# Kernel optimization log

Hardware: AMD Instinct MI355X
Metric: run time of the kernel (lower is better)

## Reference

```python
import jax, jax.numpy as jnp
import numpy as np

B, N, IN, OUT, H = 256, 131, 512, 1024, 4
D = OUT // H  # head_dim
EDGE_SCALE = D ** -0.5
NODE_SCALE = OUT ** -0.5

lrelu = lambda x: jax.nn.leaky_relu(x, negative_slope=0.01)


def _glorot(key, shape):
    fan_in = shape[-1]
    return jax.random.normal(key, shape, dtype=jnp.float32) * (1.0 / np.sqrt(fan_in))


def setup_inputs() -> dict:
    key = jax.random.key(0)
    ks = jax.random.split(key, 16)
    return {
        "tabular_feats": jax.random.normal(ks[0], (B, 1, IN), dtype=jnp.float32),
        "node_feats": jax.random.normal(ks[1], (B, N, IN), dtype=jnp.float32),
        "adj_matrix": jax.random.uniform(ks[2], (B, N, N), dtype=jnp.float32),
        "W_gx": _glorot(ks[3], (OUT, IN)), "b_gx": jnp.zeros((OUT,), jnp.float32),
        "W_tx": _glorot(ks[4], (OUT, IN)), "b_tx": jnp.zeros((OUT,), jnp.float32),
        "W_gk": _glorot(ks[5], (OUT, IN)),
        "W_tq": _glorot(ks[6], (OUT, IN)),
        "W_gq": _glorot(ks[7], (OUT, IN)),
        "W_gs": _glorot(ks[8], (1, N)), "b_gs": jnp.zeros((1,), jnp.float32),
        "W_zx": _glorot(ks[9], (OUT, 2 * OUT)), "b_zx": jnp.zeros((OUT,), jnp.float32),
    }


def preprocess_adj(A):
    # add self-loops then symmetric degree normalization D^{-1/2} (A+I) D^{-1/2}
    A = A + jnp.eye(A.shape[-1], dtype=A.dtype)
    d_inv = jax.lax.rsqrt(jnp.sum(A, axis=-1))  # [b,h,x]
    return d_inv[..., :, None] * A * d_inv[..., None, :]


def reference(tabular_feats, node_feats, adj_matrix,
              W_gx, b_gx, W_tx, b_tx, W_gk, W_tq, W_gq, W_gs, b_gs, W_zx, b_zx):
    G_X = lrelu(node_feats @ W_gx.T + b_gx)            # [B,N,OUT]
    T_X = lrelu(tabular_feats @ W_tx.T + b_tx)         # [B,1,OUT]
    G_k = lrelu(node_feats @ W_gk.T)                   # [B,N,OUT]
    T_q = lrelu(tabular_feats @ W_tq.T)                # [B,1,OUT]

    node_att = jax.nn.softmax(jnp.einsum('bxh,byh->bxy', T_q, G_k) * NODE_SCALE, axis=-1)
    node_att = jnp.swapaxes(node_att + 1.0, -1, -2)    # [B,N,1]
    G_X = node_att * G_X                               # [B,N,OUT]

    G_X_mh = G_X.reshape(B, N, H, D).transpose(0, 2, 1, 3)            # [B,H,N,D]
    G_q_mh = lrelu(node_feats @ W_gq.T).reshape(B, N, H, D).transpose(0, 2, 1, 3)
    G_k_mh = G_k.reshape(B, N, H, D).transpose(0, 2, 1, 3)

    edge_att = jax.nn.sigmoid(jnp.einsum('bhxd,bhyd->bhxy', G_q_mh, G_k_mh) * EDGE_SCALE)
    adj_heads = adj_matrix[:, None] * edge_att         # [B,H,N,N]
    A = preprocess_adj(adj_heads)

    G_X = jnp.einsum('bhxy,bhyd->bhxd', A, G_X_mh).transpose(0, 2, 1, 3).reshape(B, N, OUT)

    # Graph_summary: Linear(num_node -> 1) over the node axis
    global_node = lrelu(jnp.einsum('bno,n->bo', G_X, W_gs[0]) + b_gs)  # [B,OUT]
    Z_in = jnp.concatenate([global_node, T_X.reshape(B, -1)], axis=-1)  # [B,2*OUT]
    Z_x = lrelu(Z_in @ W_zx.T + b_zx)                  # [B,OUT]
    return (G_X, T_X, Z_x, node_att, edge_att)
```

## Files before the change

### kernel.cpp

```cpp
#include <hip/hip_runtime.h>
#include <hip/hip_bf16.h>
#include <math.h>


#define LRELU(x) ((x) > 0.f ? (x) : 0.01f * (x))

constexpr int Bb = 256;
constexpr int Nn = 131;
constexpr int INF_ = 512;
constexpr int OUTF = 1024;
constexpr int Hh = 4;
constexpr int Dd = 256;
constexpr int OC2 = 2048;
constexpr int YP = 168;
constexpr int WLP = 174;
constexpr int KAGG = 160;

typedef __attribute__((ext_vector_type(8))) short bf16x8;
typedef __attribute__((ext_vector_type(4))) float f32x4;

__device__ __forceinline__ float bf2f(short s) {
    union { float f; unsigned u; } c;
    c.u = ((unsigned)(unsigned short)s) << 16;
    return c.f;
}

__device__ __forceinline__ void gload_lds16(const void* g, void* lds) {
    __builtin_amdgcn_global_load_lds(
        (const __attribute__((address_space(1))) void*)g,
        (__attribute__((address_space(3))) void*)lds, 16, 0, 0);
}

__global__ __launch_bounds__(256) void convert_kernel(
    const float* __restrict__ node, const float* __restrict__ Wgx,
    const float* __restrict__ Wgk, const float* __restrict__ Wgq,
    __hip_bfloat16* __restrict__ node_bf, __hip_bfloat16* __restrict__ Wcat)
{
    const size_t NE = (size_t)Bb * Nn * INF_ / 4;
    const size_t WE = (size_t)3072 * INF_ / 4;
    for (size_t i = (size_t)blockIdx.x * 256 + threadIdx.x; i < NE + WE;
         i += (size_t)gridDim.x * 256) {
        if (i < NE) {
            const float4 v = ((const float4*)node)[i];
            __hip_bfloat16* o = node_bf + i * 4;
            o[0] = __float2bfloat16(v.x); o[1] = __float2bfloat16(v.y);
            o[2] = __float2bfloat16(v.z); o[3] = __float2bfloat16(v.w);
        } else {
            const size_t j = i - NE;
            const size_t which = j / (1024 * INF_ / 4);
            const float* src = (which == 0) ? Wgk : (which == 1 ? Wgq : Wgx);
            const size_t srcj = j - which * (1024 * INF_ / 4);
            const float4 v = ((const float4*)src)[srcj];
            __hip_bfloat16* o = Wcat + j * 4;
            o[0] = __float2bfloat16(v.x); o[1] = __float2bfloat16(v.y);
            o[2] = __float2bfloat16(v.z); o[3] = __float2bfloat16(v.w);
        }
    }
}

__global__ __launch_bounds__(256, 4) void gemm_node_mfma(
    const __hip_bfloat16* __restrict__ A, const __hip_bfloat16* __restrict__ W,
    const float* __restrict__ bias_gx, const float* __restrict__ Tq,
    __hip_bfloat16* __restrict__ Gcat, __hip_bfloat16* __restrict__ GrawT,
    float* __restrict__ spart)
{
    __shared__ short SM[16384];
    short* As = SM;
    short* Bs = SM + 8192;
    const int tid = threadIdx.x;
    const int wave = tid >> 6, lane = tid & 63;
    const int m0 = blockIdx.y * 128, o0 = blockIdx.x * 128;
    const int wr = wave >> 1, wc = wave & 1;

    f32x4 acc[4][4] = {};
    const short* Asrc = (const short*)A;
    const short* Wsrc = (const short*)W;
    const int gsrc = ((tid & 7) ^ ((tid >> 3) & 7)) * 8;
    const int srow = tid >> 3;

    for (int kt = 0; kt < 8; ++kt) {
        const int k0 = kt * 64;
        #pragma unroll
        for (int j = 0; j < 4; ++j) {
            const int row = j * 32 + srow;
            gload_lds16(Asrc + (size_t)(m0 + row) * INF_ + k0 + gsrc,
                        &As[(j * 256 + (tid & ~63)) * 8]);
            gload_lds16(Wsrc + (size_t)(o0 + row) * INF_ + k0 + gsrc,
                        &Bs[(j * 256 + (tid & ~63)) * 8]);
        }
        __syncthreads();
        #pragma unroll
        for (int ks = 0; ks < 2; ++ks) {
            const int sa = ((ks * 4 + (lane >> 4)) ^ (lane & 7)) * 8;
            bf16x8 af[4], bfr[4];
            #pragma unroll
            for (int i = 0; i < 4; ++i) {
                af[i]  = *(const bf16x8*)&As[(wr * 64 + i * 16 + (lane & 15)) * 64 + sa];
                bfr[i] = *(const bf16x8*)&Bs[(wc * 64 + i * 16 + (lane & 15)) * 64 + sa];
            }
            #pragma unroll
            for (int mi = 0; mi < 4; ++mi)
                #pragma unroll
                for (int ni = 0; ni < 4; ++ni)
                    acc[mi][ni] = __builtin_amdgcn_mfma_f32_16x16x32_bf16(
                        af[mi], bfr[ni], acc[mi][ni], 0, 0, 0);
        }
        __syncthreads();
    }

    const int cc = lane & 15;
    const int rg = (lane >> 4) * 4;
    if (o0 < 1024) {
        const int blo = m0 / 131;
        const int msw = (blo + 1) * 131;
        float tqA[4], tqB[4];
        #pragma unroll
        for (int ni = 0; ni < 4; ++ni) {
            const int o = o0 + wc * 64 + ni * 16 + cc;
            tqA[ni] = Tq[(size_t)blo * OUTF + o];
            tqB[ni] = (blo + 1 < Bb) ? Tq[(size_t)(blo + 1) * OUTF + o] : 0.f;
        }
        float sc[4][4] = {};
        #pragma unroll
        for (int mi = 0; mi < 4; ++mi)
            #pragma unroll
            for (int ni = 0; ni < 4; ++ni) {
                const int o = o0 + wc * 64 + ni * 16 + cc;
                #pragma unroll
                for (int r = 0; r < 4; ++r) {
                    const int m = m0 + wr * 64 + mi * 16 + rg + r;
                    float v = acc[mi][ni][r];
                    v = LRELU(v);
                    Gcat[(size_t)m * OC2 + o] = __float2bfloat16(v);
                    sc[mi][r] += v * ((m >= msw) ? tqB[ni] : tqA[ni]);
                }
            }
        const int slot = (o0 >> 6) + wc;
        #pragma unroll
        for (int mi = 0; mi < 4; ++mi)
            #pragma unroll
            for (int r = 0; r < 4; ++r) {
                float s = sc[mi][r];
                s += __shfl_xor(s, 1); s += __shfl_xor(s, 2);
                s += __shfl_xor(s, 4); s += __shfl_xor(s, 8);
                if (cc == 0) {
                    const int m = m0 + wr * 64 + mi * 16 + rg + r;
                    spart[(size_t)m * 16 + slot] = s;
                }
            }
    } else if (o0 < OC2) {
        #pragma unroll
        for (int mi = 0; mi < 4; ++mi)
            #pragma unroll
            for (int ni = 0; ni < 4; ++ni) {
                const int o = o0 + wc * 64 + ni * 16 + cc;
                #pragma unroll
                for (int r = 0; r < 4; ++r) {
                    const int m = m0 + wr * 64 + mi * 16 + rg + r;
                    float v = acc[mi][ni][r];
                    v = LRELU(v);
                    Gcat[(size_t)m * OC2 + o] = __float2bfloat16(v);
                }
            }
    } else {
        const int og0 = o0 - OC2;
        const int h = og0 >> 8;
        const int dbase = og0 & 255;
        __syncthreads();
        #pragma unroll
        for (int mi = 0; mi < 4; ++mi)
            #pragma unroll
            for (int ni = 0; ni < 4; ++ni) {
                const int dloc = wc * 64 + ni * 16 + cc;
                const float badd = bias_gx[og0 + dloc];
                #pragma unroll
                for (int r = 0; r < 4; ++r) {
                    const int row = wr * 64 + mi * 16 + rg + r;
                    float v = acc[mi][ni][r] + badd;
                    v = LRELU(v);
                    __hip_bfloat16 hb = __float2bfloat16(v);
                    const int g = row >> 3;
                    SM[dloc * 128 + ((g ^ (dloc & 7)) << 3) + (row & 7)] = *(short*)&hb;
                }
            }
        __syncthreads();
        short* GT = (short*)GrawT;
        #pragma unroll
        for (int j = 0; j < 8; ++j) {
            const int task = j * 256 + tid;
            const int dloc = task >> 4;
            const int g = task & 15;
            const bf16x8 v = *(const bf16x8*)&SM[dloc * 128 + ((g ^ (dloc & 7)) << 3)];
            const int m = m0 + g * 8;
            const int gd = dbase + dloc;
            const int b0 = m / 131;
            const int n0 = m - b0 * 131;
            if (n0 + 8 <= Nn) {
                *(bf16x8*)&GT[((size_t)(b0 * Hh + h) * 256 + gd) * YP + n0] = v;
            } else {
                #pragma unroll
                for (int e = 0; e < 8; ++e) {
                    const int mm = m + e;
                    const int bb = mm / 131;
                    const int nn = mm - bb * 131;
                    GT[((size_t)(bb * Hh + h) * 256 + gd) * YP + nn] = ((const short*)&v)[e];
                }
            }
        }
    }
}

__global__ __launch_bounds__(256) void gemm_tab(
    const float* __restrict__ Atab, const float* __restrict__ Wtx,
    const float* __restrict__ btx, const float* __restrict__ Wtq,
    float* __restrict__ Ctx, float* __restrict__ Ctq)
{
    const int which = blockIdx.x >> 4;
    const float* Wm = which ? Wtq : Wtx;
    float* C = which ? Ctq : Ctx;
    __shared__ float As[16][68];
    __shared__ float Ws[16][68];
    const int tid = threadIdx.x;
    const int tx = tid & 15;
    const int ty = tid >> 4;
    const int m0 = blockIdx.y * 64;
    const int o0 = (blockIdx.x & 15) * 64;

    float acc[4][4] = {};
    for (int k0 = 0; k0 < INF_; k0 += 16) {
        const int j = tid & 15;
        const int i = tid >> 4;
        #pragma unroll
        for (int r = 0; r < 4; ++r)
            As[j][i + 16 * r] = Atab[(size_t)(m0 + i + 16 * r) * INF_ + k0 + j];
        #pragma unroll
        for (int r = 0; r < 4; ++r)
            Ws[j][i + 16 * r] = Wm[(size_t)(o0 + i + 16 * r) * INF_ + k0 + j];
        __syncthreads();
        #pragma unroll
        for (int kk = 0; kk < 16; ++kk) {
            const float4 av = *(const float4*)&As[kk][ty * 4];
            const float4 wv = *(const float4*)&Ws[kk][tx * 4];
            const float a[4] = {av.x, av.y, av.z, av.w};
            const float w[4] = {wv.x, wv.y, wv.z, wv.w};
            #pragma unroll
            for (int r = 0; r < 4; ++r)
                #pragma unroll
                for (int c = 0; c < 4; ++c)
                    acc[r][c] += a[r] * w[c];
        }
        __syncthreads();
    }
    #pragma unroll
    for (int r = 0; r < 4; ++r) {
        const int m = m0 + ty * 4 + r;
        const int o = o0 + tx * 4;
        float4 v;
        float* vp = (float*)&v;
        #pragma unroll
        for (int c = 0; c < 4; ++c) {
            float t = acc[r][c] + (which ? 0.f : btx[o + c]);
            vp[c] = LRELU(t);
        }
        *(float4*)&C[(size_t)m * OUTF + o] = v;
    }
}

__global__ __launch_bounds__(256) void zin_build(
    const float* __restrict__ gnode, const float* __restrict__ bgs,
    const float* __restrict__ Tx, float* __restrict__ Zin)
{
    const int idx = blockIdx.x * 256 + threadIdx.x;
    const int b = idx >> 10, o = idx & 1023;
    const float s = gnode[idx] + bgs[0];
    Zin[(size_t)b * 2048 + o] = LRELU(s);
    Zin[(size_t)b * 2048 + 1024 + o] = Tx[idx];
}

__global__ __launch_bounds__(256) void gemm_zsplit(
    const float* __restrict__ A, const float* __restrict__ W,
    float* __restrict__ P)
{
    __shared__ float As[16][68];
    __shared__ float Ws[16][68];
    const int tid = threadIdx.x;
    const int tx = tid & 15;
    const int ty = tid >> 4;
    const int m0 = blockIdx.y * 64;
    const int o0 = blockIdx.x * 64;
    const int kbase = blockIdx.z * 512;

    float acc[4][4] = {};
    for (int k0 = kbase; k0 < kbase + 512; k0 += 16) {
        const int j = tid & 15;
        const int i = tid >> 4;
        #pragma unroll
        for (int r = 0; r < 4; ++r)
            As[j][i + 16 * r] = A[(size_t)(m0 + i + 16 * r) * 2048 + k0 + j];
        #pragma unroll
        for (int r = 0; r < 4; ++r)
            Ws[j][i + 16 * r] = W[(size_t)(o0 + i + 16 * r) * 2048 + k0 + j];
        __syncthreads();
        #pragma unroll
        for (int kk = 0; kk < 16; ++kk) {
            const float4 av = *(const float4*)&As[kk][ty * 4];
            const float4 wv = *(const float4*)&Ws[kk][tx * 4];
            const float a[4] = {av.x, av.y, av.z, av.w};
            const float w[4] = {wv.x, wv.y, wv.z, wv.w};
            #pragma unroll
            for (int r = 0; r < 4; ++r)
                #pragma unroll
                for (int c = 0; c < 4; ++c)
                    acc[r][c] += a[r] * w[c];
        }
        __syncthreads();
    }
    float* pz = P + (size_t)blockIdx.z * Bb * OUTF;
    #pragma unroll
    for (int r = 0; r < 4; ++r) {
        const int m = m0 + ty * 4 + r;
        const int o = o0 + tx * 4;
        float4 v;
        float* vp = (float*)&v;
        #pragma unroll
        for (int c = 0; c < 4; ++c) vp[c] = acc[r][c];
        *(float4*)&pz[(size_t)m * OUTF + o] = v;
    }
}

__global__ __launch_bounds__(256) void zreduce(
    const float* __restrict__ P, const float* __restrict__ bzx,
    float* __restrict__ C)
{
    const int idx = blockIdx.x * 256 + threadIdx.x;
    const int o = idx & 1023;
    const size_t STRIDE = (size_t)Bb * OUTF;
    float s = P[idx] + P[STRIDE + idx] + P[2 * STRIDE + idx] + P[3 * STRIDE + idx]
            + bzx[o];
    C[idx] = LRELU(s);
}

__global__ __launch_bounds__(256) void nodeatt_soft(
    const float* __restrict__ spart, float* __restrict__ att)
{
    const int b = blockIdx.x;
    __shared__ float sc[136];
    const int tid = threadIdx.x;
    if (tid < Nn) {
        const float* sp = spart + (size_t)(b * Nn + tid) * 16;
        float s = 0.f;
        #pragma unroll
        for (int i = 0; i < 16; ++i) s += sp[i];
        sc[tid] = s * (1.f / 32.f);
    }
    __syncthreads();
    if (tid < 64) {
        const float v1 = sc[tid];
        const float v2 = sc[tid + 64];
        const float v3 = (tid < 3) ? sc[tid + 128] : -1e30f;
        float m = fmaxf(fmaxf(v1, v2), v3);
        #pragma unroll
        for (int off = 32; off; off >>= 1) m = fmaxf(m, __shfl_xor(m, off));
        const float e1 = expf(v1 - m);
        const float e2 = expf(v2 - m);
        const float e3 = (tid < 3) ? expf(v3 - m) : 0.f;
        float s = e1 + e2 + e3;
        #pragma unroll
        for (int off = 32; off; off >>= 1) s += __shfl_xor(s, off);
        const float inv = 1.f / s;
        float* ab = att + (size_t)b * Nn;
        ab[tid] = e1 * inv + 1.f;
        ab[tid + 64] = e2 * inv + 1.f;
        if (tid < 3) ab[tid + 128] = e3 * inv + 1.f;
    }
}

__global__ __launch_bounds__(576) void edge_agg(
    const __hip_bfloat16* __restrict__ Gcat, const float* __restrict__ adj,
    const float* __restrict__ att, const __hip_bfloat16* __restrict__ GrawT,
    const float* __restrict__ Wgs, float* __restrict__ edge,
    float* __restrict__ Gout, float* __restrict__ gnode)
{
    __shared__ short SM[25056];
    __shared__ float rsL[144 * 3];
    __shared__ float dxL[Nn], daL[Nn], attL[Nn], wgsL[Nn];

    const int bh = blockIdx.x, b = bh >> 2, h = bh & 3;
    const int tid = threadIdx.x;
    const int lane = tid & 63, wid = tid >> 6;
    const int wr = wid / 3, wc = wid % 3;
    if (tid < Nn) { attL[tid] = att[(size_t)b * Nn + tid]; wgsL[tid] = Wgs[tid]; }

    const short* qb = (const short*)Gcat + (size_t)b * Nn * OC2 + 1024 + h * Dd;
    const short* kb = (const short*)Gcat + (size_t)b * Nn * OC2 + h * Dd;
    const short* gsrcT = (const short*)GrawT + (size_t)bh * 256 * YP;
    const float* adjb = adj + (size_t)b * Nn * Nn;

    int srow = tid >> 2; if (srow > Nn - 1) srow = Nn - 1;
    const int gsrc = ((tid & 3) ^ ((tid >> 3) & 3)) * 8;
    const int dstoff = (tid & ~63) * 8;
    const int cc = lane & 15;
    const int rg = (lane >> 4) * 4;

    float areg[3][3][4];
    #pragma unroll
    for (int mi = 0; mi < 3; ++mi)
        #pragma unroll
        for (int ni = 0; ni < 3; ++ni) {
            const int y = wc * 48 + ni * 16 + cc;
            #pragma unroll
            for (int r = 0; r < 4; ++r) {
                const int x = wr * 48 + mi * 16 + rg + r;
                areg[mi][ni][r] = (x < Nn && y < Nn) ? adjb[x * Nn + y] : 0.f;
            }
        }

    auto STAGE = [&](int buf, int k0) {
        gload_lds16(qb + (size_t)srow * OC2 + k0 + gsrc, &SM[buf * 4608 + dstoff]);
        gload_lds16(kb + (size_t)srow * OC2 + k0 + gsrc, &SM[9216 + buf * 4608 + dstoff]);
    };

    f32x4 acc[3][3] = {};
    const int sa = ((lane >> 4) ^ ((lane >> 1) & 3)) * 8;

    STAGE(0, 0);
    for (int t = 0; t < 8; ++t) {
        const int buf = t & 1;
        if (t < 7) {
            STAGE(buf ^ 1, (t + 1) * 32);
            asm volatile("s_waitcnt vmcnt(2)" ::: "memory");
        } else {
            asm volatile("s_waitcnt vmcnt(0)" ::: "memory");
        }
        __builtin_amdgcn_s_barrier();
        __builtin_amdgcn_sched_barrier(0);
        bf16x8 qf[3], kf[3];
        #pragma unroll
        for (int i = 0; i < 3; ++i) {
            qf[i] = *(const bf16x8*)&SM[buf * 4608 + (wr * 48 + i * 16 + (lane & 15)) * 32 + sa];
            kf[i] = *(const bf16x8*)&SM[9216 + buf * 4608 + (wc * 48 + i * 16 + (lane & 15)) * 32 + sa];
        }
        __builtin_amdgcn_s_setprio(1);
        #pragma unroll
        for (int mi = 0; mi < 3; ++mi)
            #pragma unroll
            for (int ni = 0; ni < 3; ++ni)
                acc[mi][ni] = __builtin_amdgcn_mfma_f32_16x16x32_bf16(
                    qf[mi], kf[ni], acc[mi][ni], 0, 0, 0);
        __builtin_amdgcn_s_setprio(0);
        __builtin_amdgcn_sched_barrier(0);
        if (t < 7) __builtin_amdgcn_s_barrier();
    }

    const int brow0 = wid * 32 + (lane & 15);
    const int bcol = (lane >> 4) * 8;
    bf16x8 bcur0, bcur1;
    if (wid < 8) {
        bcur0 = *(const bf16x8*)&gsrcT[(size_t)brow0 * YP + 0 + bcol];
        bcur1 = *(const bf16x8*)&gsrcT[(size_t)(brow0 + 16) * YP + 0 + bcol];
    }

    float* edgeb = edge + (size_t)bh * Nn * Nn;
    #pragma unroll
    for (int mi = 0; mi < 3; ++mi) {
        float rsum[4] = {0.f, 0.f, 0.f, 0.f};
        #pragma unroll
        for (int ni = 0; ni < 3; ++ni) {
            const int y = wc * 48 + ni * 16 + cc;
            #pragma unroll
            for (int r = 0; r < 4; ++r) {
                const int x = wr * 48 + mi * 16 + rg + r;
                const bool in = (x < Nn) && (y < Nn);
                const float e = 1.f / (1.f + __expf(-acc[mi][ni][r] * (1.f / 16.f)));
                acc[mi][ni][r] = e;
                if (in) {
                    edgeb[x * Nn + y] = e;
                    rsum[r] += areg[mi][ni][r] * e;
                }
            }
        }
        #pragma unroll
        for (int r = 0; r < 4; ++r) {
            float v = rsum[r];
            v += __shfl_xor(v, 1); v += __shfl_xor(v, 2);
            v += __shfl_xor(v, 4); v += __shfl_xor(v, 8);
            const int x = wr * 48 + mi * 16 + rg + r;
            if (cc == 0 && x < Nn) rsL[x * 3 + wc] = v;
        }
    }
    __syncthreads();
    if (tid < Nn) {
        const float s = rsL[tid * 3] + rsL[tid * 3 + 1] + rsL[tid * 3 + 2];
        const float dv = rsqrtf(s + 1.f);
        dxL[tid] = dv;
        daL[tid] = dv * attL[tid];
    }
    __syncthreads();

    short* WbL = SM;
    for (int i = tid; i < 144 * 29; i += 576) {
        const int x = i / 29, y = 131 + i % 29;
        WbL[x * WLP + y] = 0;
    }
    #pragma unroll
    for (int mi = 0; mi < 3; ++mi)
        #pragma unroll
        for (int ni = 0; ni < 3; ++ni) {
            const int y = wc * 48 + ni * 16 + cc;
            #pragma unroll
            for (int r = 0; r < 4; ++r) {
                const int x = wr * 48 + mi * 16 + rg + r;
                if (x < Nn && y < Nn) {
                    float a = areg[mi][ni][r] * acc[mi][ni][r];
                    if (x == y) a += 1.f;
                    const float w = dxL[x] * a * daL[y];
                    __hip_bfloat16 hb = __float2bfloat16(w);
                    WbL[(size_t)x * WLP + y] = *(short*)&hb;
                }
            }
        }
    __syncthreads();

    if (wid < 8) {
        f32x4 gacc[9][2] = {};
        #pragma unroll
        for (int kc = 0; kc < 5; ++kc) {
            bf16x8 bnxt0, bnxt1;
            if (kc < 4) {
                bnxt0 = *(const bf16x8*)&gsrcT[(size_t)brow0 * YP + (kc + 1) * 32 + bcol];
                bnxt1 = *(const bf16x8*)&gsrcT[(size_t)(brow0 + 16) * YP + (kc + 1) * 32 + bcol];
            }
            bf16x8 af[9];
            #pragma unroll
            for (int mi = 0; mi < 9; ++mi)
                af[mi] = *(const bf16x8*)&WbL[(mi * 16 + (lane & 15)) * WLP + kc * 32 + (lane >> 4) * 8];
            __builtin_amdgcn_s_setprio(1);
            #pragma unroll
            for (int mi = 0; mi < 9; ++mi) {
                gacc[mi][0] = __builtin_amdgcn_mfma_f32_16x16x32_bf16(
                    af[mi], bcur0, gacc[mi][0], 0, 0, 0);
                gacc[mi][1] = __builtin_amdgcn_mfma_f32_16x16x32_bf16(
                    af[mi], bcur1, gacc[mi][1], 0, 0, 0);
            }
            __builtin_amdgcn_s_setprio(0);
            if (kc < 4) { bcur0 = bnxt0; bcur1 = bnxt1; }
        }

        float* gob = Gout + (size_t)b * Nn * OUTF + h * Dd;
        float gp[2] = {0.f, 0.f};
        #pragma unroll
        for (int mi = 0; mi < 9; ++mi)
            #pragma unroll
            for (int ni = 0; ni < 2; ++ni) {
                const int d = wid * 32 + ni * 16 + (lane & 15);
                #pragma unroll
                for (int r = 0; r < 4; ++r) {
                    const int x = mi * 16 + (lane >> 4) * 4 + r;
                    if (x < Nn) {
                        gob[(size_t)x * OUTF + d] = gacc[mi][ni][r];
                        gp[ni] += wgsL[x] * gacc[mi][ni][r];
                    }
                }
            }
        #pragma unroll
        for (int ni = 0; ni < 2; ++ni) {
            gp[ni] += __shfl_xor(gp[ni], 16);
            gp[ni] += __shfl_xor(gp[ni], 32);
            if (lane < 16)
                gnode[(size_t)b * OUTF + h * Dd + wid * 32 + ni * 16 + lane] = gp[ni];
        }
    }
}

extern "C" void kernel_launch(void* const* d_in, const int* in_sizes, int n_in,
                              void* d_out, int out_size, void* d_ws, size_t ws_size,
                              hipStream_t stream) {
    const float* tab  = (const float*)d_in[0];
    const float* node = (const float*)d_in[1];
    const float* adj  = (const float*)d_in[2];
    const float* W_gx = (const float*)d_in[3];
    const float* b_gx = (const float*)d_in[4];
    const float* W_tx = (const float*)d_in[5];
    const float* b_tx = (const float*)d_in[6];
    const float* W_gk = (const float*)d_in[7];
    const float* W_tq = (const float*)d_in[8];
    const float* W_gq = (const float*)d_in[9];
    const float* W_gs = (const float*)d_in[10];
    const float* b_gs = (const float*)d_in[11];
    const float* W_zx = (const float*)d_in[12];
    const float* b_zx = (const float*)d_in[13];

    const size_t GX_ELEMS = (size_t)Bb * Nn * OUTF;
    const int M_NODE = Bb * Nn;

    float* out   = (float*)d_out;
    float* o_GX  = out;
    float* o_TX  = o_GX + GX_ELEMS;
    float* o_ZX  = o_TX + (size_t)Bb * OUTF;
    float* o_ATT = o_ZX + (size_t)Bb * OUTF;
    float* o_EDG = o_ATT + (size_t)Bb * Nn;

    __hip_bfloat16* wb      = (__hip_bfloat16*)d_ws;
    __hip_bfloat16* w_nodeb = wb;
    __hip_bfloat16* w_Wcat  = w_nodeb + (size_t)M_NODE * INF_;
    __hip_bfloat16* w_Gcat  = w_Wcat + (size_t)3072 * INF_;
    __hip_bfloat16* w_GrawT = w_Gcat + (size_t)M_NODE * OC2;
    float* wf       = (float*)(w_GrawT + (size_t)Bb * Hh * 256 * YP);
    float* w_Tq     = wf;
    float* w_Zin    = w_Tq + (size_t)Bb * OUTF;
    float* w_gnode  = w_Zin + (size_t)Bb * 2 * OUTF;
    float* w_spart  = w_gnode + (size_t)Bb * OUTF;
    float* w_zpart  = w_spart + (size_t)M_NODE * 16;

    const dim3 blk(256);

    convert_kernel<<<dim3(2048), blk, 0, stream>>>(node, W_gx, W_gk, W_gq,
                                                   w_nodeb, w_Wcat);
    gemm_tab<<<dim3(32, 4), blk, 0, stream>>>(tab, W_tx, b_tx, W_tq, o_TX, w_Tq);
    gemm_node_mfma<<<dim3(24, M_NODE / 128), blk, 0, stream>>>(
        w_nodeb, w_Wcat, b_gx, w_Tq, w_Gcat, w_GrawT, w_spart);
    nodeatt_soft<<<dim3(Bb), blk, 0, stream>>>(w_spart, o_ATT);
    edge_agg<<<dim3(Bb * Hh), dim3(576), 0, stream>>>(
        w_Gcat, adj, o_ATT, w_GrawT, W_gs, o_EDG, o_GX, w_gnode);
    zin_build<<<dim3((Bb * OUTF) / 256), blk, 0, stream>>>(w_gnode, b_gs, o_TX, w_Zin);
    gemm_zsplit<<<dim3(16, 4, 4), blk, 0, stream>>>(w_Zin, W_zx, w_zpart);
    zreduce<<<dim3((Bb * OUTF) / 256), blk, 0, stream>>>(w_zpart, b_zx, o_ZX);
}
```

Baseline: 365.1 us.

## Split edge_agg aggregation into two column passes and request higher occupancy

The aggregation GEMM in edge_agg now handles its two 16-column output tiles one after another instead of together, which halves the live accumulator and B-fragment registers. The launch bounds now ask for 5 blocks per multiprocessor so the compiler caps register use. The trade-off is that the A fragments from shared memory are read twice, once per column tile, and the early B prefetch that overlapped the sigmoid phase is gone. Tighter register limits could also cause spills in the first MFMA phase.

```diff
diff --git a/kernel.cpp b/kernel.cpp
--- a/kernel.cpp
+++ b/kernel.cpp
@@ -375,7 +375,7 @@
     }
 }
 
-__global__ __launch_bounds__(576) void edge_agg(
+__global__ __launch_bounds__(576, 5) void edge_agg(
     const __hip_bfloat16* __restrict__ Gcat, const float* __restrict__ adj,
     const float* __restrict__ att, const __hip_bfloat16* __restrict__ GrawT,
     const float* __restrict__ Wgs, float* __restrict__ edge,
@@ -452,14 +452,6 @@
         if (t < 7) __builtin_amdgcn_s_barrier();
     }
 
-    const int brow0 = wid * 32 + (lane & 15);
-    const int bcol = (lane >> 4) * 8;
-    bf16x8 bcur0, bcur1;
-    if (wid < 8) {
-        bcur0 = *(const bf16x8*)&gsrcT[(size_t)brow0 * YP + 0 + bcol];
-        bcur1 = *(const bf16x8*)&gsrcT[(size_t)(brow0 + 16) * YP + 0 + bcol];
-    }
-
     float* edgeb = edge + (size_t)bh * Nn * Nn;
     #pragma unroll
     for (int mi = 0; mi < 3; ++mi) {
@@ -522,52 +514,46 @@
     __syncthreads();
 
     if (wid < 8) {
-        f32x4 gacc[9][2] = {};
-        #pragma unroll
-        for (int kc = 0; kc < 5; ++kc) {
-            bf16x8 bnxt0, bnxt1;
-            if (kc < 4) {
-                bnxt0 = *(const bf16x8*)&gsrcT[(size_t)brow0 * YP + (kc + 1) * 32 + bcol];
-                bnxt1 = *(const bf16x8*)&gsrcT[(size_t)(brow0 + 16) * YP + (kc + 1) * 32 + bcol];
-            }
-            bf16x8 af[9];
+        float* gob = Gout + (size_t)b * Nn * OUTF + h * Dd;
+        const int bcol = (lane >> 4) * 8;
+        #pragma unroll
+        for (int ni = 0; ni < 2; ++ni) {
+            const int brow = wid * 32 + ni * 16 + (lane & 15);
+            bf16x8 bcur = *(const bf16x8*)&gsrcT[(size_t)brow * YP + 0 + bcol];
+            f32x4 gacc[9] = {};
+            #pragma unroll
+            for (int kc = 0; kc < 5; ++kc) {
+                bf16x8 bnxt;
+                if (kc < 4)
+                    bnxt = *(const bf16x8*)&gsrcT[(size_t)brow * YP + (kc + 1) * 32 + bcol];
+                bf16x8 af[9];
+                #pragma unroll
+                for (int mi = 0; mi < 9; ++mi)
+                    af[mi] = *(const bf16x8*)&WbL[(mi * 16 + (lane & 15)) * WLP + kc * 32 + (lane >> 4) * 8];
+                __builtin_amdgcn_s_setprio(1);
+                #pragma unroll
+                for (int mi = 0; mi < 9; ++mi)
+                    gacc[mi] = __builtin_amdgcn_mfma_f32_16x16x32_bf16(
+                        af[mi], bcur, gacc[mi], 0, 0, 0);
+                __builtin_amdgcn_s_setprio(0);
+                if (kc < 4) bcur = bnxt;
+            }
+            const int d = wid * 32 + ni * 16 + (lane & 15);
+            float gp = 0.f;
             #pragma unroll
             for (int mi = 0; mi < 9; ++mi)
-                af[mi] = *(const bf16x8*)&WbL[(mi * 16 + (lane & 15)) * WLP + kc * 32 + (lane >> 4) * 8];
-            __builtin_amdgcn_s_setprio(1);
-            #pragma unroll
-            for (int mi = 0; mi < 9; ++mi) {
-                gacc[mi][0] = __builtin_amdgcn_mfma_f32_16x16x32_bf16(
-                    af[mi], bcur0, gacc[mi][0], 0, 0, 0);
-                gacc[mi][1] = __builtin_amdgcn_mfma_f32_16x16x32_bf16(
-                    af[mi], bcur1, gacc[mi][1], 0, 0, 0);
-            }
-            __builtin_amdgcn_s_setprio(0);
-            if (kc < 4) { bcur0 = bnxt0; bcur1 = bnxt1; }
-        }
-
-        float* gob = Gout + (size_t)b * Nn * OUTF + h * Dd;
-        float gp[2] = {0.f, 0.f};
-        #pragma unroll
-        for (int mi = 0; mi < 9; ++mi)
-            #pragma unroll
-            for (int ni = 0; ni < 2; ++ni) {
-                const int d = wid * 32 + ni * 16 + (lane & 15);
                 #pragma unroll
                 for (int r = 0; r < 4; ++r) {
                     const int x = mi * 16 + (lane >> 4) * 4 + r;
                     if (x < Nn) {
-                        gob[(size_t)x * OUTF + d] = gacc[mi][ni][r];
-                        gp[ni] += wgsL[x] * gacc[mi][ni][r];
+                        gob[(size_t)x * OUTF + d] = gacc[mi][r];
+                        gp += wgsL[x] * gacc[mi][r];
                     }
                 }
-            }
-        #pragma unroll
-        for (int ni = 0; ni < 2; ++ni) {
-            gp[ni] += __shfl_xor(gp[ni], 16);
-            gp[ni] += __shfl_xor(gp[ni], 32);
+            gp += __shfl_xor(gp, 16);
+            gp += __shfl_xor(gp, 32);
             if (lane < 16)
-                gnode[(size_t)b * OUTF + h * Dd + wid * 32 + ni * 16 + lane] = gp[ni];
+                gnode[(size_t)b * OUTF + h * Dd + d] = gp;
         }
     }
 }
```

Result: slower. 519.4 us (+42.3%).
